# Optimization experiments

Measured on AMD Instinct MI355X. Metric: run time of the kernel, lower is better.

Reference implementation:

```python
import jax, jax.numpy as jnp
import numpy as np

N, E, T, D, A = 50000, 160000, 8192, 32, 6  # nodes, edges, torsions, dim, action_dim


def setup_inputs() -> dict:
    key = jax.random.key(0)
    ks = jax.random.split(key, 16)
    rn = lambda k, s, sc=0.1: jax.random.normal(k, s, jnp.float32) * sc
    return {
        "x": jax.random.normal(ks[0], (N, 3), jnp.float32),
        "edge_index": jax.random.randint(ks[1], (2, E), 0, N),
        "edge_attr": jax.random.uniform(ks[2], (E, 7), dtype=jnp.float32),
        "nonring": jax.random.randint(ks[3], (T, 4), 0, N),
        "lin0_w": rn(ks[4], (3, D)), "lin0_b": jnp.zeros((D,), jnp.float32),
        "nn1_w": rn(ks[5], (7, D)), "nn1_b": jnp.zeros((D,), jnp.float32),
        "nn2_w": rn(ks[6], (D, D * D), 0.02), "nn2_b": jnp.zeros((D * D,), jnp.float32),
        "conv_root": rn(ks[7], (D, D)), "conv_b": jnp.zeros((D,), jnp.float32),
        "gru_w_ih": rn(ks[8], (D, 3 * D)), "gru_w_hh": rn(ks[9], (D, 3 * D)),
        "gru_b_ih": jnp.zeros((3 * D,), jnp.float32), "gru_b_hh": jnp.zeros((3 * D,), jnp.float32),
        "lstm_w_ih": rn(ks[10], (2 * D, 4 * D)), "lstm_w_hh": rn(ks[11], (D, 4 * D)),
        "lstm_b_ih": jnp.zeros((4 * D,), jnp.float32), "lstm_b_hh": jnp.zeros((4 * D,), jnp.float32),
        "lin1_w": rn(ks[12], (6 * D, D)), "lin1_b": jnp.zeros((D,), jnp.float32),
        "lin2_w": rn(ks[13], (D, A)), "lin2_b": jnp.zeros((A,), jnp.float32),
    }


def reference(x, edge_index, edge_attr, nonring,
              lin0_w, lin0_b, nn1_w, nn1_b, nn2_w, nn2_b, conv_root, conv_b,
              gru_w_ih, gru_w_hh, gru_b_ih, gru_b_hh,
              lstm_w_ih, lstm_w_hh, lstm_b_ih, lstm_b_hh,
              lin1_w, lin1_b, lin2_w, lin2_b):
    src, dst = edge_index[0], edge_index[1]
    out = jax.nn.relu(x @ lin0_w + lin0_b)                       # [N, D]
    h = out                                                      # GRU hidden (batch = nodes)
    # Per-edge dim x dim weight matrices (edge_attr is loop-invariant)
    Wedge = (jax.nn.relu(edge_attr @ nn1_w + nn1_b) @ nn2_w + nn2_b).reshape(E, D, D)
    deg = jnp.clip(jax.ops.segment_sum(jnp.ones((E,), jnp.float32), dst, num_segments=N), 1.0)[:, None]
    for _ in range(6):
        # NNConv: gather -> per-edge matvec -> scatter-mean, plus root transform + bias
        msg = jnp.einsum('ei,eio->eo', out[src], Wedge)          # [E, D]
        agg = jax.ops.segment_sum(msg, dst, num_segments=N) / deg
        m = jax.nn.relu(out @ conv_root + agg + conv_b)
        # GRU step (torch gate order r, z, n)
        gx = m @ gru_w_ih + gru_b_ih
        gh = h @ gru_w_hh + gru_b_hh
        r = jax.nn.sigmoid(gx[:, :D] + gh[:, :D])
        z = jax.nn.sigmoid(gx[:, D:2 * D] + gh[:, D:2 * D])
        n = jnp.tanh(gx[:, 2 * D:] + r * gh[:, 2 * D:])
        h = (1.0 - z) * n + z * h
        out = h
    # Set2Set pooling, single graph (B = 1); torch LSTM gate order i, f, g, o
    hl = jnp.zeros((D,), out.dtype)
    cl = jnp.zeros((D,), out.dtype)
    q_star = jnp.zeros((2 * D,), out.dtype)
    for _ in range(6):
        g = q_star @ lstm_w_ih + lstm_b_ih + hl @ lstm_w_hh + lstm_b_hh
        i = jax.nn.sigmoid(g[:D]); f = jax.nn.sigmoid(g[D:2 * D])
        gg = jnp.tanh(g[2 * D:3 * D]); o = jax.nn.sigmoid(g[3 * D:])
        cl = f * cl + i * gg
        hl = o * jnp.tanh(cl)
        q = hl
        a = jax.nn.softmax(out @ q)                              # attention over all nodes
        r_vec = a @ out                                          # [D]
        q_star = jnp.concatenate([q, r_vec])                     # [2D]
    pool = q_star                                                # [2D]
    g4 = out[nonring.reshape(-1)]                                # [4T, D]
    g4 = g4.reshape(4 * D, -1).T                                 # [T, 4D] (faithful view+permute)
    rep = jnp.repeat(pool, g4.shape[0]).reshape(g4.shape[0], -1) # [T, 2D] (repeat_interleave+view)
    cat = jnp.concatenate([g4, rep], axis=1)                     # [T, 6D]
    y = jax.nn.relu(cat @ lin1_w + lin1_b)
    return y @ lin2_w + lin2_b                                   # [T, A]
```

## Files before the change

### kernel.cpp

```cpp
#include <hip/hip_runtime.h>
#include <hip/hip_bf16.h>

#define NN 50000
#define NE 160000
#define NT 8192
#define DD 32
#define AA 6

typedef __attribute__((ext_vector_type(8))) short bf16x8s;
typedef __attribute__((ext_vector_type(4))) float f32x4;

__device__ float g_out[NN * DD];
__device__ float g_msg[NE * DD];
__device__ unsigned int g_h2b[NE * 16];
__device__ int g_src[NE];
__device__ int g_poe[NE];
__device__ unsigned int g_bcnt[NN];
__device__ unsigned int g_row[NN + 1];
__device__ unsigned int g_cur[NN];
__device__ unsigned int g_btot[256], g_boff[256];
__device__ bf16x8s g_w2frag[33 * 2 * 64];
__device__ bf16x8s g_gru_frag[28 * 64];
__device__ float g_hl[DD], g_cl[DD], g_q[DD], g_part[DD + 1];
__device__ unsigned int g_cnt;

__device__ __forceinline__ float sigm(float x) { return 1.0f / (1.0f + __expf(-x)); }
__device__ __forceinline__ float tanhx(float x) { return 1.0f - 2.0f / (__expf(2.0f * x) + 1.0f); }
__device__ __forceinline__ unsigned short f2bf(float f) {
    unsigned int u = __float_as_uint(f);
    u = (u + 0x7fffu + ((u >> 16) & 1u)) >> 16;
    return (unsigned short)u;
}
__device__ __forceinline__ float bflo(unsigned int pk) { return __uint_as_float(pk << 16); }
__device__ __forceinline__ float bfhi(unsigned int pk) { return __uint_as_float(pk & 0xffff0000u); }
__device__ __forceinline__ void fma4(float4& a, float s, const float4 b) {
    a.x = fmaf(s, b.x, a.x); a.y = fmaf(s, b.y, a.y);
    a.z = fmaf(s, b.z, a.z); a.w = fmaf(s, b.w, a.w);
}
#define CVTPK(dst, lo, hi) asm("v_cvt_pk_bf16_f32 %0, %1, %2" : "=v"(dst) : "v"(lo), "v"(hi))

__device__ __forceinline__ void split8(const float* v, bf16x8s& hi, bf16x8s& lo) {
    union U { bf16x8s v; unsigned int u[4]; } H, L;
    CVTPK(H.u[0], v[0], v[1]); CVTPK(H.u[1], v[2], v[3]);
    CVTPK(H.u[2], v[4], v[5]); CVTPK(H.u[3], v[6], v[7]);
    float r[8];
#pragma unroll
    for (int q = 0; q < 4; ++q) {
        r[2 * q]     = v[2 * q]     - bflo(H.u[q]);
        r[2 * q + 1] = v[2 * q + 1] - bfhi(H.u[q]);
    }
    CVTPK(L.u[0], r[0], r[1]); CVTPK(L.u[1], r[2], r[3]);
    CVTPK(L.u[2], r[4], r[5]); CVTPK(L.u[3], r[6], r[7]);
    hi = H.v; lo = L.v;
}

__global__ __launch_bounds__(256) void k_zero() {
    const int n = blockIdx.x * 256 + threadIdx.x;
    if (n < NN) g_bcnt[n] = 0u;
}

__global__ __launch_bounds__(256) void k_hist(const int* __restrict__ ei) {
    const int e = blockIdx.x * 256 + threadIdx.x;
    atomicAdd(&g_bcnt[ei[NE + e]], 1u);
}

__global__ __launch_bounds__(256) void k_scanA() {
    __shared__ unsigned int s[256];
    const int t = threadIdx.x;
    const int idx = blockIdx.x * 256 + t;
    const unsigned int c = (idx < NN) ? g_bcnt[idx] : 0u;
    s[t] = c;
    __syncthreads();
#pragma unroll
    for (int off = 1; off < 256; off <<= 1) {
        const unsigned int o = (t >= off) ? s[t - off] : 0u;
        __syncthreads();
        s[t] += o;
        __syncthreads();
    }
    if (idx < NN) g_row[idx] = s[t] - c;
    if (t == 255) g_btot[blockIdx.x] = s[255];
}

__global__ void k_scanB() {
    __shared__ unsigned int s[256];
    const int t = threadIdx.x;
    const unsigned int c = (t < 196) ? g_btot[t] : 0u;
    s[t] = c;
    __syncthreads();
#pragma unroll
    for (int off = 1; off < 256; off <<= 1) {
        const unsigned int o = (t >= off) ? s[t - off] : 0u;
        __syncthreads();
        s[t] += o;
        __syncthreads();
    }
    if (t < 196) g_boff[t] = s[t] - c;
}

__global__ __launch_bounds__(256) void k_scanC() {
    const int idx = blockIdx.x * 256 + threadIdx.x;
    if (idx < NN) {
        const unsigned int v = g_row[idx] + g_boff[blockIdx.x];
        g_row[idx] = v;
        g_cur[idx] = v;
    }
    if (idx == 0) g_row[NN] = NE;
}

__global__ __launch_bounds__(256) void k_scatter(const int* __restrict__ ei) {
    const int e = blockIdx.x * 256 + threadIdx.x;
    const int d = ei[NE + e];
    const unsigned int pos = atomicAdd(&g_cur[d], 1u);
    g_src[pos] = ei[e];
    g_poe[pos] = e;
}

__global__ __launch_bounds__(256) void k_init(const float* __restrict__ x,
                                              const float* __restrict__ w,
                                              const float* __restrict__ b) {
    const int t = blockIdx.x * 256 + threadIdx.x;
    const int n = t >> 5, d = t & 31;
    float v = b[d];
    v = fmaf(x[n * 3 + 0], w[0 * DD + d], v);
    v = fmaf(x[n * 3 + 1], w[1 * DD + d], v);
    v = fmaf(x[n * 3 + 2], w[2 * DD + d], v);
    g_out[t] = fmaxf(v, 0.f);
}

__global__ __launch_bounds__(256) void k_h2(const float* __restrict__ ea,
                                            const float* __restrict__ w,
                                            const float* __restrict__ b) {
    const int t = blockIdx.x * 256 + threadIdx.x;
    const int p = t >> 4, kp = t & 15;
    const int oe = g_poe[p];
    const int k0 = kp * 2;
    float a0 = b[k0], a1 = b[k0 + 1];
#pragma unroll
    for (int i = 0; i < 7; ++i) {
        const float eav = ea[oe * 7 + i];
        a0 = fmaf(eav, w[i * DD + k0], a0);
        a1 = fmaf(eav, w[i * DD + k0 + 1], a1);
    }
    unsigned int pk;
    CVTPK(pk, fmaxf(a0, 0.f), fmaxf(a1, 0.f));
    g_h2b[t] = pk;
}

__global__ __launch_bounds__(256) void k_w2frag(const float* __restrict__ w2m,
                                                const float* __restrict__ b2m) {
    const int idx = blockIdx.x * 256 + threadIdx.x;
    const int j = idx & 7, l = (idx >> 3) & 63, c = (idx >> 9) & 1, s = idx >> 10;
    const int kk = (l >> 4) * 8 + j;
    const int col = c * 16 + (l & 15);
    const float v = (s == 32) ? b2m[kk * DD + col] : w2m[(32 * s + kk) * DD + col];
    ((unsigned short*)g_w2frag)[idx] = f2bf(v);
}

__global__ __launch_bounds__(256) void k_gfrag(const float* __restrict__ root,
                                               const float* __restrict__ wih,
                                               const float* __restrict__ whh) {
    const int tid = blockIdx.x * 256 + threadIdx.x;
    if (tid >= 28 * 64) return;
    const int lane = tid & 63, f = tid >> 6;
    const float* M; int ncols, c, part;
    if (f < 4)       { M = root; ncols = 32; c = f >> 1;        part = f & 1; }
    else if (f < 16) { M = wih;  ncols = 96; c = (f - 4) >> 1;  part = f & 1; }
    else             { M = whh;  ncols = 96; c = (f - 16) >> 1; part = f & 1; }
    unsigned short out8[8];
#pragma unroll
    for (int j = 0; j < 8; ++j) {
        const int k = (lane >> 4) * 8 + j;
        const float v = M[k * ncols + c * 16 + (lane & 15)];
        const unsigned short hi = f2bf(v);
        out8[j] = (part == 0) ? hi : f2bf(v - __uint_as_float((unsigned int)hi << 16));
    }
    g_gru_frag[f * 64 + lane] = *(bf16x8s*)out8;
}

__global__ __launch_bounds__(256) void k_edge_mfma() {
    const int wid = threadIdx.x >> 6, lane = threadIdx.x & 63;
    const int w = blockIdx.x * 4 + wid;
    const int col = lane & 15, quad = lane >> 4;
    const bf16x8s* __restrict__ B = g_w2frag;

    const bf16x8s bbias0 = B[32 * 128 + lane];
    const bf16x8s bbias1 = B[32 * 128 + 64 + lane];

    float4 u0[2], u1[2];
    unsigned int h2p[2][16];
#pragma unroll
    for (int g = 0; g < 2; ++g) {
        const int e = w * 32 + g * 16 + col;
        const int src = g_src[e];
        u0[g] = *(const float4*)&g_out[src * DD + quad * 8];
        u1[g] = *(const float4*)&g_out[src * DD + quad * 8 + 4];
        *(uint4*)&h2p[g][0]  = *(const uint4*)&g_h2b[e * 16];
        *(uint4*)&h2p[g][4]  = *(const uint4*)&g_h2b[e * 16 + 4];
        *(uint4*)&h2p[g][8]  = *(const uint4*)&g_h2b[e * 16 + 8];
        *(uint4*)&h2p[g][12] = *(const uint4*)&g_h2b[e * 16 + 12];
    }

    union ABu { bf16x8s v; unsigned int u[4]; };
    f32x4 acc[2][2];
#pragma unroll
    for (int g = 0; g < 2; ++g) {
        acc[g][0] = (f32x4){0.f, 0.f, 0.f, 0.f};
        acc[g][1] = (f32x4){0.f, 0.f, 0.f, 0.f};
    }

#define EDGE_STEP(S, B0V, B1V)                                                                   \
    do {                                                                                          \
        _Pragma("unroll")                                                                         \
        for (int g = 0; g < 2; ++g) {                                                             \
            const unsigned int hw = h2p[g][(S) >> 1];                                             \
            const float hs = ((S)&1) ? bfhi(hw) : bflo(hw);                                       \
            ABu A;                                                                                \
            CVTPK(A.u[0], hs * u0[g].x, hs * u0[g].y);                                            \
            CVTPK(A.u[1], hs * u0[g].z, hs * u0[g].w);                                            \
            CVTPK(A.u[2], hs * u1[g].x, hs * u1[g].y);                                            \
            CVTPK(A.u[3], hs * u1[g].z, hs * u1[g].w);                                            \
            acc[g][0] = __builtin_amdgcn_mfma_f32_16x16x32_bf16(A.v, B0V, acc[g][0], 0, 0, 0);    \
            acc[g][1] = __builtin_amdgcn_mfma_f32_16x16x32_bf16(A.v, B1V, acc[g][1], 0, 0, 0);    \
        }                                                                                         \
    } while (0)

    bf16x8s ca0 = B[0 * 128 + lane], cb0 = B[0 * 128 + 64 + lane];
    bf16x8s ca1 = B[1 * 128 + lane], cb1 = B[1 * 128 + 64 + lane];
    bf16x8s ca2 = B[2 * 128 + lane], cb2 = B[2 * 128 + 64 + lane];
    bf16x8s ca3 = B[3 * 128 + lane], cb3 = B[3 * 128 + 64 + lane];
    bf16x8s na0, nb0, na1, nb1, na2, nb2, na3, nb3;

#pragma unroll
    for (int blk = 0; blk < 8; ++blk) {
        if (blk < 7) {
            const int r = blk * 4 + 4;
            na0 = B[(r + 0) * 128 + lane]; nb0 = B[(r + 0) * 128 + 64 + lane];
            na1 = B[(r + 1) * 128 + lane]; nb1 = B[(r + 1) * 128 + 64 + lane];
            na2 = B[(r + 2) * 128 + lane]; nb2 = B[(r + 2) * 128 + 64 + lane];
            na3 = B[(r + 3) * 128 + lane]; nb3 = B[(r + 3) * 128 + 64 + lane];
        }
        EDGE_STEP(blk * 4 + 0, ca0, cb0);
        EDGE_STEP(blk * 4 + 1, ca1, cb1);
        EDGE_STEP(blk * 4 + 2, ca2, cb2);
        EDGE_STEP(blk * 4 + 3, ca3, cb3);
        if (blk < 7) {
            ca0 = na0; cb0 = nb0; ca1 = na1; cb1 = nb1;
            ca2 = na2; cb2 = nb2; ca3 = na3; cb3 = nb3;
        }
    }
#undef EDGE_STEP

    {
#pragma unroll
        for (int g = 0; g < 2; ++g) {
            ABu Au;
            CVTPK(Au.u[0], u0[g].x, u0[g].y); CVTPK(Au.u[1], u0[g].z, u0[g].w);
            CVTPK(Au.u[2], u1[g].x, u1[g].y); CVTPK(Au.u[3], u1[g].z, u1[g].w);
            acc[g][0] = __builtin_amdgcn_mfma_f32_16x16x32_bf16(Au.v, bbias0, acc[g][0], 0, 0, 0);
            acc[g][1] = __builtin_amdgcn_mfma_f32_16x16x32_bf16(Au.v, bbias1, acc[g][1], 0, 0, 0);
        }
    }
#pragma unroll
    for (int g = 0; g < 2; ++g)
#pragma unroll
        for (int r = 0; r < 4; ++r) {
            const int p = w * 32 + g * 16 + quad * 4 + r;
            g_msg[p * DD + col] = acc[g][0][r];
            g_msg[p * DD + 16 + col] = acc[g][1][r];
        }
}

__global__ __launch_bounds__(256) void k_node_mfma(const float* __restrict__ cb,
                                                   const float* __restrict__ bih,
                                                   const float* __restrict__ bhh) {
    __shared__ float sm[4][16 * 36];
    const int wid = threadIdx.x >> 6, lane = threadIdx.x & 63;
    const int nt = blockIdx.x * 4 + wid;
    if (nt >= NN / 16) return;
    const int nb = nt * 16;
    const int col = lane & 15, quad = lane >> 4;
    const bf16x8s* FB = g_gru_frag;

    float hv8[8];
    *(float4*)&hv8[0] = *(const float4*)&g_out[(nb + col) * DD + quad * 8];
    *(float4*)&hv8[4] = *(const float4*)&g_out[(nb + col) * DD + quad * 8 + 4];
    bf16x8s hAh, hAl; split8(hv8, hAh, hAl);

    float aggv0[4], aggv1[4], invr[4];
#pragma unroll
    for (int r = 0; r < 4; ++r) {
        const int node = nb + quad * 4 + r;
        const unsigned int e0 = g_row[node], e1 = g_row[node + 1];
        float a0 = 0.f, a1 = 0.f;
        for (unsigned int e = e0; e < e1; ++e) {
            a0 += g_msg[e * DD + col];
            a1 += g_msg[e * DD + 16 + col];
        }
        aggv0[r] = a0; aggv1[r] = a1;
        invr[r] = 1.0f / fmaxf((float)(e1 - e0), 1.0f);
    }

#pragma unroll
    for (int c = 0; c < 2; ++c) {
        const float cbv = cb[c * 16 + col];
        f32x4 aM;
#pragma unroll
        for (int r = 0; r < 4; ++r)
            aM[r] = fmaf((c == 0) ? aggv0[r] : aggv1[r], invr[r], cbv);
        const bf16x8s Bh = FB[(c * 2 + 0) * 64 + lane];
        const bf16x8s Bl = FB[(c * 2 + 1) * 64 + lane];
        aM = __builtin_amdgcn_mfma_f32_16x16x32_bf16(hAh, Bh, aM, 0, 0, 0);
        aM = __builtin_amdgcn_mfma_f32_16x16x32_bf16(hAl, Bh, aM, 0, 0, 0);
        aM = __builtin_amdgcn_mfma_f32_16x16x32_bf16(hAh, Bl, aM, 0, 0, 0);
#pragma unroll
        for (int r = 0; r < 4; ++r)
            sm[wid][(quad * 4 + r) * 36 + c * 16 + col] = fmaxf(aM[r], 0.f);
    }

    float mv8[8];
    *(float4*)&mv8[0] = *(const float4*)&sm[wid][col * 36 + quad * 8];
    *(float4*)&mv8[4] = *(const float4*)&sm[wid][col * 36 + quad * 8 + 4];
    bf16x8s mAh, mAl; split8(mv8, mAh, mAl);

    f32x4 R[2], Z[2], XN[2], HN[2];
#pragma unroll
    for (int c = 0; c < 6; ++c) {
        const float bx = bih[c * 16 + col], bh = bhh[c * 16 + col];
        f32x4 aX = {bx, bx, bx, bx}, aH = {bh, bh, bh, bh};
        const bf16x8s WIhf = FB[(4 + c * 2) * 64 + lane];
        const bf16x8s WIlf = FB[(5 + c * 2) * 64 + lane];
        const bf16x8s WHhf = FB[(16 + c * 2) * 64 + lane];
        const bf16x8s WHlf = FB[(17 + c * 2) * 64 + lane];
        aX = __builtin_amdgcn_mfma_f32_16x16x32_bf16(mAh, WIhf, aX, 0, 0, 0);
        aX = __builtin_amdgcn_mfma_f32_16x16x32_bf16(mAl, WIhf, aX, 0, 0, 0);
        aX = __builtin_amdgcn_mfma_f32_16x16x32_bf16(mAh, WIlf, aX, 0, 0, 0);
        aH = __builtin_amdgcn_mfma_f32_16x16x32_bf16(hAh, WHhf, aH, 0, 0, 0);
        aH = __builtin_amdgcn_mfma_f32_16x16x32_bf16(hAl, WHhf, aH, 0, 0, 0);
        aH = __builtin_amdgcn_mfma_f32_16x16x32_bf16(hAh, WHlf, aH, 0, 0, 0);
        if (c < 2) {
#pragma unroll
            for (int r = 0; r < 4; ++r) R[c][r] = sigm(aX[r] + aH[r]);
        } else if (c < 4) {
#pragma unroll
            for (int r = 0; r < 4; ++r) Z[c - 2][r] = sigm(aX[r] + aH[r]);
        } else {
            XN[c - 4] = aX; HN[c - 4] = aH;
        }
    }
#pragma unroll
    for (int c = 0; c < 2; ++c)
#pragma unroll
        for (int r = 0; r < 4; ++r) {
            const int addr = (nb + quad * 4 + r) * DD + c * 16 + col;
            const float nv = tanhx(XN[c][r] + R[c][r] * HN[c][r]);
            const float hv = g_out[addr];
            g_out[addr] = (1.f - Z[c][r]) * nv + Z[c][r] * hv;
        }
}

__global__ void k_lstm0(const float* __restrict__ bih, const float* __restrict__ bhh) {
    __shared__ float gg[128];
    const int t = threadIdx.x;
    gg[t] = bih[t] + bhh[t];
    __syncthreads();
    if (t < DD) {
        const float ig = sigm(gg[t]), fg = sigm(gg[DD + t]);
        const float g2 = tanhx(gg[2 * DD + t]), og = sigm(gg[3 * DD + t]);
        const float cc = ig * g2;
        g_cl[t] = cc; const float hn = og * tanhx(cc); g_hl[t] = hn; g_q[t] = hn;
        (void)fg;
    }
    if (t >= DD && t < 2 * DD + 1) g_part[t - DD] = 0.f;
    if (t == 0) g_cnt = 0u;
}

__global__ __launch_bounds__(256) void k_att_f(const float* __restrict__ wih,
                                               const float* __restrict__ whh,
                                               const float* __restrict__ bih,
                                               const float* __restrict__ bhh,
                                               const int dolstm) {
    __shared__ float sq[DD];
    __shared__ float red[4][DD + 1];
    __shared__ int slast;
    __shared__ float qs[64], shl[DD], gg[128];
    if (threadIdx.x < DD) sq[threadIdx.x] = g_q[threadIdx.x];
    __syncthreads();
    float pe = 0.f;
    float pv[DD];
#pragma unroll
    for (int i = 0; i < DD; ++i) pv[i] = 0.f;
    for (int n = blockIdx.x * blockDim.x + threadIdx.x; n < NN; n += gridDim.x * blockDim.x) {
        float row[DD];
#pragma unroll
        for (int q = 0; q < 8; ++q) *(float4*)&row[4 * q] = *(const float4*)&g_out[n * DD + 4 * q];
        float dot = 0.f;
#pragma unroll
        for (int i = 0; i < DD; ++i) dot = fmaf(row[i], sq[i], dot);
        const float e = __expf(dot);
        pe += e;
#pragma unroll
        for (int i = 0; i < DD; ++i) pv[i] = fmaf(e, row[i], pv[i]);
    }
#pragma unroll
    for (int off = 32; off > 0; off >>= 1) {
        pe += __shfl_down(pe, off, 64);
#pragma unroll
        for (int i = 0; i < DD; ++i) pv[i] += __shfl_down(pv[i], off, 64);
    }
    const int wid = threadIdx.x >> 6, lane = threadIdx.x & 63;
    if (lane == 0) {
        red[wid][0] = pe;
#pragma unroll
        for (int i = 0; i < DD; ++i) red[wid][1 + i] = pv[i];
    }
    __syncthreads();
    if (threadIdx.x < DD + 1) {
        const float s = red[0][threadIdx.x] + red[1][threadIdx.x] + red[2][threadIdx.x] + red[3][threadIdx.x];
        atomicAdd(&g_part[threadIdx.x], s);
    }
    __threadfence();
    __syncthreads();
    if (threadIdx.x == 0) {
        const unsigned int o = atomicAdd(&g_cnt, 1u);
        slast = (o == (unsigned int)(gridDim.x - 1)) ? 1 : 0;
    }
    __syncthreads();
    if (!slast) return;
    __threadfence();
    const int t = threadIdx.x;
    if (dolstm) {
        if (t < DD) { qs[t] = g_q[t]; shl[t] = g_hl[t]; }
        else if (t < 64) qs[t] = g_part[1 + t - DD] / g_part[0];
        __syncthreads();
        if (t < 128) {
            float acc = bih[t] + bhh[t];
            for (int i = 0; i < 64; ++i) acc = fmaf(qs[i], wih[i * 128 + t], acc);
            for (int i = 0; i < DD; ++i) acc = fmaf(shl[i], whh[i * 128 + t], acc);
            gg[t] = acc;
        }
        __syncthreads();
        if (t < DD) {
            const float ig = sigm(gg[t]), fg = sigm(gg[DD + t]);
            const float g2 = tanhx(gg[2 * DD + t]), og = sigm(gg[3 * DD + t]);
            const float cc = fmaf(fg, g_cl[t], ig * g2);
            g_cl[t] = cc; const float hn = og * tanhx(cc); g_hl[t] = hn; g_q[t] = hn;
        }
        if (t >= DD && t < 2 * DD + 1) g_part[t - DD] = 0.f;
    }
    if (t == 0) g_cnt = 0u;
}

__global__ __launch_bounds__(128) void k_readout(const int* __restrict__ nr,
                                                 const float* __restrict__ w1,
                                                 const float* __restrict__ b1,
                                                 const float* __restrict__ w2,
                                                 const float* __restrict__ b2,
                                                 float* __restrict__ yout) {
    __shared__ float sw1[192 * DD];
    __shared__ float sS1[DD];
    __shared__ float sw2[DD * AA];
    __shared__ float sb1[DD];
    __shared__ float sb2[AA];
    __shared__ float sred[32 * DD];
    for (int i = threadIdx.x; i < 192 * DD; i += 128) sw1[i] = w1[i];
    for (int i = threadIdx.x; i < DD * AA; i += 128) sw2[i] = w2[i];
    if (threadIdx.x < DD) sb1[threadIdx.x] = b1[threadIdx.x];
    if (threadIdx.x >= DD && threadIdx.x < DD + AA) sb2[threadIdx.x - DD] = b2[threadIdx.x - DD];
    __syncthreads();
    if (threadIdx.x < DD) {
        float s = 0.f;
        for (int c = 0; c < 64; ++c) s += sw1[(128 + c) * DD + threadIdx.x];
        sS1[threadIdx.x] = s;
    }
    __syncthreads();
    const int g = blockIdx.x;
    const int t0 = g * 32;
    const int f = threadIdx.x & 31;
    const int slice = threadIdx.x >> 5;
    const int rowbase = g >> 2, col = g & 3;
    float4 acc[8];
#pragma unroll
    for (int q = 0; q < 8; ++q) acc[q] = make_float4(0.f, 0.f, 0.f, 0.f);
    for (int pp = 0; pp < 32; ++pp) {
        const int p = slice * 32 + pp;
        const int node = nr[(p * 64 + rowbase) * 4 + col];
        const float v = g_out[node * DD + f];
#pragma unroll
        for (int q = 0; q < 8; ++q) fma4(acc[q], v, *(const float4*)&sw1[p * DD + 4 * q]);
    }
#pragma unroll
    for (int q = 0; q < 8; ++q) {
        acc[q].x += __shfl_xor(acc[q].x, 32, 64);
        acc[q].y += __shfl_xor(acc[q].y, 32, 64);
        acc[q].z += __shfl_xor(acc[q].z, 32, 64);
        acc[q].w += __shfl_xor(acc[q].w, 32, 64);
    }
    if (threadIdx.x >= 64 && threadIdx.x < 96) {
#pragma unroll
        for (int q = 0; q < 8; ++q) *(float4*)&sred[f * DD + 4 * q] = acc[q];
    }
    __syncthreads();
    if (threadIdx.x < 32) {
        const int pidx = g >> 2;
        const float poolv = (pidx < DD) ? g_q[pidx] : (g_part[1 + (pidx - DD)] / g_part[0]);
        float y[AA];
#pragma unroll
        for (int a = 0; a < AA; ++a) y[a] = sb2[a];
#pragma unroll
        for (int q = 0; q < 8; ++q) {
            const float4 o = *(const float4*)&sred[f * DD + 4 * q];
            const float vals[4] = {acc[q].x + o.x, acc[q].y + o.y, acc[q].z + o.z, acc[q].w + o.w};
#pragma unroll
            for (int cc = 0; cc < 4; ++cc) {
                const int d = 4 * q + cc;
                const float ad = fmaxf(fmaf(poolv, sS1[d], sb1[d]) + vals[cc], 0.f);
#pragma unroll
                for (int a = 0; a < AA; ++a) y[a] = fmaf(ad, sw2[d * AA + a], y[a]);
            }
        }
#pragma unroll
        for (int a = 0; a < AA; ++a) yout[(t0 + f) * AA + a] = y[a];
    }
}

extern "C" void kernel_launch(void* const* d_in, const int* in_sizes, int n_in,
                              void* d_out, int out_size, void* d_ws, size_t ws_size,
                              hipStream_t stream) {
    (void)in_sizes; (void)n_in; (void)out_size; (void)d_ws; (void)ws_size;
    const float* x        = (const float*)d_in[0];
    const int*   ei       = (const int*)d_in[1];
    const float* ea       = (const float*)d_in[2];
    const int*   nonring  = (const int*)d_in[3];
    const float* lin0_w   = (const float*)d_in[4];
    const float* lin0_b   = (const float*)d_in[5];
    const float* nn1_w    = (const float*)d_in[6];
    const float* nn1_b    = (const float*)d_in[7];
    const float* nn2_w    = (const float*)d_in[8];
    const float* nn2_b    = (const float*)d_in[9];
    const float* conv_root= (const float*)d_in[10];
    const float* conv_b   = (const float*)d_in[11];
    const float* gru_w_ih = (const float*)d_in[12];
    const float* gru_w_hh = (const float*)d_in[13];
    const float* gru_b_ih = (const float*)d_in[14];
    const float* gru_b_hh = (const float*)d_in[15];
    const float* lstm_w_ih= (const float*)d_in[16];
    const float* lstm_w_hh= (const float*)d_in[17];
    const float* lstm_b_ih= (const float*)d_in[18];
    const float* lstm_b_hh= (const float*)d_in[19];
    const float* lin1_w   = (const float*)d_in[20];
    const float* lin1_b   = (const float*)d_in[21];
    const float* lin2_w   = (const float*)d_in[22];
    const float* lin2_b   = (const float*)d_in[23];
    float* out = (float*)d_out;

    k_zero<<<196, 256, 0, stream>>>();
    k_hist<<<NE / 256, 256, 0, stream>>>(ei);
    k_scanA<<<196, 256, 0, stream>>>();
    k_scanB<<<1, 256, 0, stream>>>();
    k_scanC<<<196, 256, 0, stream>>>();
    k_scatter<<<NE / 256, 256, 0, stream>>>(ei);

    k_init<<<(NN * DD) / 256, 256, 0, stream>>>(x, lin0_w, lin0_b);
    k_h2<<<(NE * 16) / 256, 256, 0, stream>>>(ea, nn1_w, nn1_b);
    k_w2frag<<<132, 256, 0, stream>>>(nn2_w, nn2_b);
    k_gfrag<<<7, 256, 0, stream>>>(conv_root, gru_w_ih, gru_w_hh);
    for (int it = 0; it < 6; ++it) {
        k_edge_mfma<<<1250, 256, 0, stream>>>();
        k_node_mfma<<<(NN / 16 + 3) / 4, 256, 0, stream>>>(conv_b, gru_b_ih, gru_b_hh);
    }
    k_lstm0<<<1, 128, 0, stream>>>(lstm_b_ih, lstm_b_hh);
    for (int s = 0; s < 6; ++s) {
        k_att_f<<<196, 256, 0, stream>>>(lstm_w_ih, lstm_w_hh, lstm_b_ih, lstm_b_hh, (s < 5) ? 1 : 0);
    }
    k_readout<<<256, 128, 0, stream>>>(nonring, lin1_w, lin1_b, lin2_w, lin2_b, out);
}
```

Before: 440.6 us.

## Fuse edge message computation into node GRU kernel with ping-pong node buffers

Merges the per-edge NNConv message MFMA kernel into the per-node aggregation/GRU kernel. Each wave now walks the CSR edge range of its 16-node tile in chunks of 16 edges, computes messages into LDS and accumulates them directly, which removes the global g_msg write and read each iteration. Because messages now read node state while other blocks update it, the node state is double-buffered (g_out/g_out2) with the iteration parity picking the buffers. The trade-off is fewer waves and less independent work per wave, one edge group instead of two, and idle lanes in partial chunks.

Measured after the change: 649.7 us. +47.5%, slower.

```diff
diff --git a/kernel.cpp b/kernel.cpp
--- a/kernel.cpp
+++ b/kernel.cpp
@@ -11,7 +11,7 @@
 typedef __attribute__((ext_vector_type(4))) float f32x4;
 
 __device__ float g_out[NN * DD];
-__device__ float g_msg[NE * DD];
+__device__ float g_out2[NN * DD];
 __device__ unsigned int g_h2b[NE * 16];
 __device__ int g_src[NE];
 __device__ int g_poe[NE];
@@ -178,128 +178,123 @@
     g_gru_frag[f * 64 + lane] = *(bf16x8s*)out8;
 }
 
-__global__ __launch_bounds__(256) void k_edge_mfma() {
-    const int wid = threadIdx.x >> 6, lane = threadIdx.x & 63;
-    const int w = blockIdx.x * 4 + wid;
-    const int col = lane & 15, quad = lane >> 4;
-    const bf16x8s* __restrict__ B = g_w2frag;
-
-    const bf16x8s bbias0 = B[32 * 128 + lane];
-    const bf16x8s bbias1 = B[32 * 128 + 64 + lane];
-
-    float4 u0[2], u1[2];
-    unsigned int h2p[2][16];
-#pragma unroll
-    for (int g = 0; g < 2; ++g) {
-        const int e = w * 32 + g * 16 + col;
-        const int src = g_src[e];
-        u0[g] = *(const float4*)&g_out[src * DD + quad * 8];
-        u1[g] = *(const float4*)&g_out[src * DD + quad * 8 + 4];
-        *(uint4*)&h2p[g][0]  = *(const uint4*)&g_h2b[e * 16];
-        *(uint4*)&h2p[g][4]  = *(const uint4*)&g_h2b[e * 16 + 4];
-        *(uint4*)&h2p[g][8]  = *(const uint4*)&g_h2b[e * 16 + 8];
-        *(uint4*)&h2p[g][12] = *(const uint4*)&g_h2b[e * 16 + 12];
-    }
-
-    union ABu { bf16x8s v; unsigned int u[4]; };
-    f32x4 acc[2][2];
-#pragma unroll
-    for (int g = 0; g < 2; ++g) {
-        acc[g][0] = (f32x4){0.f, 0.f, 0.f, 0.f};
-        acc[g][1] = (f32x4){0.f, 0.f, 0.f, 0.f};
-    }
-
-#define EDGE_STEP(S, B0V, B1V)                                                                   \
-    do {                                                                                          \
-        _Pragma("unroll")                                                                         \
-        for (int g = 0; g < 2; ++g) {                                                             \
-            const unsigned int hw = h2p[g][(S) >> 1];                                             \
-            const float hs = ((S)&1) ? bfhi(hw) : bflo(hw);                                       \
-            ABu A;                                                                                \
-            CVTPK(A.u[0], hs * u0[g].x, hs * u0[g].y);                                            \
-            CVTPK(A.u[1], hs * u0[g].z, hs * u0[g].w);                                            \
-            CVTPK(A.u[2], hs * u1[g].x, hs * u1[g].y);                                            \
-            CVTPK(A.u[3], hs * u1[g].z, hs * u1[g].w);                                            \
-            acc[g][0] = __builtin_amdgcn_mfma_f32_16x16x32_bf16(A.v, B0V, acc[g][0], 0, 0, 0);    \
-            acc[g][1] = __builtin_amdgcn_mfma_f32_16x16x32_bf16(A.v, B1V, acc[g][1], 0, 0, 0);    \
-        }                                                                                         \
-    } while (0)
-
-    bf16x8s ca0 = B[0 * 128 + lane], cb0 = B[0 * 128 + 64 + lane];
-    bf16x8s ca1 = B[1 * 128 + lane], cb1 = B[1 * 128 + 64 + lane];
-    bf16x8s ca2 = B[2 * 128 + lane], cb2 = B[2 * 128 + 64 + lane];
-    bf16x8s ca3 = B[3 * 128 + lane], cb3 = B[3 * 128 + 64 + lane];
-    bf16x8s na0, nb0, na1, nb1, na2, nb2, na3, nb3;
-
-#pragma unroll
-    for (int blk = 0; blk < 8; ++blk) {
-        if (blk < 7) {
-            const int r = blk * 4 + 4;
-            na0 = B[(r + 0) * 128 + lane]; nb0 = B[(r + 0) * 128 + 64 + lane];
-            na1 = B[(r + 1) * 128 + lane]; nb1 = B[(r + 1) * 128 + 64 + lane];
-            na2 = B[(r + 2) * 128 + lane]; nb2 = B[(r + 2) * 128 + 64 + lane];
-            na3 = B[(r + 3) * 128 + lane]; nb3 = B[(r + 3) * 128 + 64 + lane];
-        }
-        EDGE_STEP(blk * 4 + 0, ca0, cb0);
-        EDGE_STEP(blk * 4 + 1, ca1, cb1);
-        EDGE_STEP(blk * 4 + 2, ca2, cb2);
-        EDGE_STEP(blk * 4 + 3, ca3, cb3);
-        if (blk < 7) {
-            ca0 = na0; cb0 = nb0; ca1 = na1; cb1 = nb1;
-            ca2 = na2; cb2 = nb2; ca3 = na3; cb3 = nb3;
-        }
-    }
-#undef EDGE_STEP
-
-    {
-#pragma unroll
-        for (int g = 0; g < 2; ++g) {
-            ABu Au;
-            CVTPK(Au.u[0], u0[g].x, u0[g].y); CVTPK(Au.u[1], u0[g].z, u0[g].w);
-            CVTPK(Au.u[2], u1[g].x, u1[g].y); CVTPK(Au.u[3], u1[g].z, u1[g].w);
-            acc[g][0] = __builtin_amdgcn_mfma_f32_16x16x32_bf16(Au.v, bbias0, acc[g][0], 0, 0, 0);
-            acc[g][1] = __builtin_amdgcn_mfma_f32_16x16x32_bf16(Au.v, bbias1, acc[g][1], 0, 0, 0);
-        }
-    }
-#pragma unroll
-    for (int g = 0; g < 2; ++g)
-#pragma unroll
-        for (int r = 0; r < 4; ++r) {
-            const int p = w * 32 + g * 16 + quad * 4 + r;
-            g_msg[p * DD + col] = acc[g][0][r];
-            g_msg[p * DD + 16 + col] = acc[g][1][r];
-        }
-}
-
-__global__ __launch_bounds__(256) void k_node_mfma(const float* __restrict__ cb,
-                                                   const float* __restrict__ bih,
-                                                   const float* __restrict__ bhh) {
+__global__ __launch_bounds__(256) void k_fused(const int it,
+                                               const float* __restrict__ cb,
+                                               const float* __restrict__ bih,
+                                               const float* __restrict__ bhh) {
     __shared__ float sm[4][16 * 36];
+    __shared__ float smsg[4][16 * 32];
     const int wid = threadIdx.x >> 6, lane = threadIdx.x & 63;
     const int nt = blockIdx.x * 4 + wid;
     if (nt >= NN / 16) return;
+    const float* __restrict__ cur = (it & 1) ? g_out2 : g_out;
+    float* __restrict__ nxt = (it & 1) ? g_out : g_out2;
     const int nb = nt * 16;
     const int col = lane & 15, quad = lane >> 4;
+    const bf16x8s* __restrict__ B = g_w2frag;
     const bf16x8s* FB = g_gru_frag;
+    float* smt = sm[wid];
+    float* smm = smsg[wid];
 
     float hv8[8];
-    *(float4*)&hv8[0] = *(const float4*)&g_out[(nb + col) * DD + quad * 8];
-    *(float4*)&hv8[4] = *(const float4*)&g_out[(nb + col) * DD + quad * 8 + 4];
+    *(float4*)&hv8[0] = *(const float4*)&cur[(nb + col) * DD + quad * 8];
+    *(float4*)&hv8[4] = *(const float4*)&cur[(nb + col) * DD + quad * 8 + 4];
     bf16x8s hAh, hAl; split8(hv8, hAh, hAl);
 
-    float aggv0[4], aggv1[4], invr[4];
+    unsigned int nr0[4], nr1[4];
 #pragma unroll
     for (int r = 0; r < 4; ++r) {
         const int node = nb + quad * 4 + r;
-        const unsigned int e0 = g_row[node], e1 = g_row[node + 1];
-        float a0 = 0.f, a1 = 0.f;
-        for (unsigned int e = e0; e < e1; ++e) {
-            a0 += g_msg[e * DD + col];
-            a1 += g_msg[e * DD + 16 + col];
-        }
-        aggv0[r] = a0; aggv1[r] = a1;
-        invr[r] = 1.0f / fmaxf((float)(e1 - e0), 1.0f);
-    }
+        nr0[r] = g_row[node];
+        nr1[r] = g_row[node + 1];
+    }
+    const unsigned int e0 = g_row[nb], e1 = g_row[nb + 16];
+
+    const bf16x8s bbias0 = B[32 * 128 + lane];
+    const bf16x8s bbias1 = B[32 * 128 + 64 + lane];
+
+    union ABu { bf16x8s v; unsigned int u[4]; };
+    float agg0[4] = {0.f, 0.f, 0.f, 0.f};
+    float agg1[4] = {0.f, 0.f, 0.f, 0.f};
+
+    for (unsigned int ec = e0; ec < e1; ec += 16) {
+        const int e = min((int)(ec + col), NE - 1);
+        const int src = g_src[e];
+        const float4 u0 = *(const float4*)&cur[src * DD + quad * 8];
+        const float4 u1 = *(const float4*)&cur[src * DD + quad * 8 + 4];
+        unsigned int h2p[16];
+        *(uint4*)&h2p[0]  = *(const uint4*)&g_h2b[(size_t)e * 16];
+        *(uint4*)&h2p[4]  = *(const uint4*)&g_h2b[(size_t)e * 16 + 4];
+        *(uint4*)&h2p[8]  = *(const uint4*)&g_h2b[(size_t)e * 16 + 8];
+        *(uint4*)&h2p[12] = *(const uint4*)&g_h2b[(size_t)e * 16 + 12];
+
+        f32x4 acc0 = {0.f, 0.f, 0.f, 0.f};
+        f32x4 acc1 = {0.f, 0.f, 0.f, 0.f};
+
+#define EDGE_STEP(S, B0V, B1V)                                                                 \
+    do {                                                                                        \
+        const unsigned int hw = h2p[(S) >> 1];                                                  \
+        const float hs = ((S)&1) ? bfhi(hw) : bflo(hw);                                         \
+        ABu A;                                                                                  \
+        CVTPK(A.u[0], hs * u0.x, hs * u0.y);                                                    \
+        CVTPK(A.u[1], hs * u0.z, hs * u0.w);                                                    \
+        CVTPK(A.u[2], hs * u1.x, hs * u1.y);                                                    \
+        CVTPK(A.u[3], hs * u1.z, hs * u1.w);                                                    \
+        acc0 = __builtin_amdgcn_mfma_f32_16x16x32_bf16(A.v, B0V, acc0, 0, 0, 0);                \
+        acc1 = __builtin_amdgcn_mfma_f32_16x16x32_bf16(A.v, B1V, acc1, 0, 0, 0);                \
+    } while (0)
+
+        bf16x8s ca0 = B[0 * 128 + lane], cb0 = B[0 * 128 + 64 + lane];
+        bf16x8s ca1 = B[1 * 128 + lane], cb1 = B[1 * 128 + 64 + lane];
+        bf16x8s ca2 = B[2 * 128 + lane], cb2 = B[2 * 128 + 64 + lane];
+        bf16x8s ca3 = B[3 * 128 + lane], cb3 = B[3 * 128 + 64 + lane];
+        bf16x8s na0, nb0, na1, nb1, na2, nb2, na3, nb3;
+#pragma unroll
+        for (int blk = 0; blk < 8; ++blk) {
+            if (blk < 7) {
+                const int r = blk * 4 + 4;
+                na0 = B[(r + 0) * 128 + lane]; nb0 = B[(r + 0) * 128 + 64 + lane];
+                na1 = B[(r + 1) * 128 + lane]; nb1 = B[(r + 1) * 128 + 64 + lane];
+                na2 = B[(r + 2) * 128 + lane]; nb2 = B[(r + 2) * 128 + 64 + lane];
+                na3 = B[(r + 3) * 128 + lane]; nb3 = B[(r + 3) * 128 + 64 + lane];
+            }
+            EDGE_STEP(blk * 4 + 0, ca0, cb0);
+            EDGE_STEP(blk * 4 + 1, ca1, cb1);
+            EDGE_STEP(blk * 4 + 2, ca2, cb2);
+            EDGE_STEP(blk * 4 + 3, ca3, cb3);
+            if (blk < 7) {
+                ca0 = na0; cb0 = nb0; ca1 = na1; cb1 = nb1;
+                ca2 = na2; cb2 = nb2; ca3 = na3; cb3 = nb3;
+            }
+        }
+#undef EDGE_STEP
+        {
+            ABu Au;
+            CVTPK(Au.u[0], u0.x, u0.y); CVTPK(Au.u[1], u0.z, u0.w);
+            CVTPK(Au.u[2], u1.x, u1.y); CVTPK(Au.u[3], u1.z, u1.w);
+            acc0 = __builtin_amdgcn_mfma_f32_16x16x32_bf16(Au.v, bbias0, acc0, 0, 0, 0);
+            acc1 = __builtin_amdgcn_mfma_f32_16x16x32_bf16(Au.v, bbias1, acc1, 0, 0, 0);
+        }
+#pragma unroll
+        for (int r = 0; r < 4; ++r) {
+            smm[(quad * 4 + r) * 32 + col] = acc0[r];
+            smm[(quad * 4 + r) * 32 + 16 + col] = acc1[r];
+        }
+#pragma unroll
+        for (int r = 0; r < 4; ++r) {
+            const int lo = (int)max(nr0[r], ec) - (int)ec;
+            const int hi = (int)min(nr1[r], ec + 16u) - (int)ec;
+            for (int s = lo; s < hi; ++s) {
+                agg0[r] += smm[s * 32 + col];
+                agg1[r] += smm[s * 32 + 16 + col];
+            }
+        }
+    }
+
+    float invr[4];
+#pragma unroll
+    for (int r = 0; r < 4; ++r)
+        invr[r] = 1.0f / fmaxf((float)(nr1[r] - nr0[r]), 1.0f);
 
 #pragma unroll
     for (int c = 0; c < 2; ++c) {
@@ -307,7 +302,7 @@
         f32x4 aM;
 #pragma unroll
         for (int r = 0; r < 4; ++r)
-            aM[r] = fmaf((c == 0) ? aggv0[r] : aggv1[r], invr[r], cbv);
+            aM[r] = fmaf((c == 0) ? agg0[r] : agg1[r], invr[r], cbv);
         const bf16x8s Bh = FB[(c * 2 + 0) * 64 + lane];
         const bf16x8s Bl = FB[(c * 2 + 1) * 64 + lane];
         aM = __builtin_amdgcn_mfma_f32_16x16x32_bf16(hAh, Bh, aM, 0, 0, 0);
@@ -315,12 +310,12 @@
         aM = __builtin_amdgcn_mfma_f32_16x16x32_bf16(hAh, Bl, aM, 0, 0, 0);
 #pragma unroll
         for (int r = 0; r < 4; ++r)
-            sm[wid][(quad * 4 + r) * 36 + c * 16 + col] = fmaxf(aM[r], 0.f);
+            smt[(quad * 4 + r) * 36 + c * 16 + col] = fmaxf(aM[r], 0.f);
     }
 
     float mv8[8];
-    *(float4*)&mv8[0] = *(const float4*)&sm[wid][col * 36 + quad * 8];
-    *(float4*)&mv8[4] = *(const float4*)&sm[wid][col * 36 + quad * 8 + 4];
+    *(float4*)&mv8[0] = *(const float4*)&smt[col * 36 + quad * 8];
+    *(float4*)&mv8[4] = *(const float4*)&smt[col * 36 + quad * 8 + 4];
     bf16x8s mAh, mAl; split8(mv8, mAh, mAl);
 
     f32x4 R[2], Z[2], XN[2], HN[2];
@@ -354,8 +349,8 @@
         for (int r = 0; r < 4; ++r) {
             const int addr = (nb + quad * 4 + r) * DD + c * 16 + col;
             const float nv = tanhx(XN[c][r] + R[c][r] * HN[c][r]);
-            const float hv = g_out[addr];
-            g_out[addr] = (1.f - Z[c][r]) * nv + Z[c][r] * hv;
+            const float hv = cur[addr];
+            nxt[addr] = (1.f - Z[c][r]) * nv + Z[c][r] * hv;
         }
 }
 
@@ -365,11 +360,10 @@
     gg[t] = bih[t] + bhh[t];
     __syncthreads();
     if (t < DD) {
-        const float ig = sigm(gg[t]), fg = sigm(gg[DD + t]);
+        const float ig = sigm(gg[t]);
         const float g2 = tanhx(gg[2 * DD + t]), og = sigm(gg[3 * DD + t]);
         const float cc = ig * g2;
         g_cl[t] = cc; const float hn = og * tanhx(cc); g_hl[t] = hn; g_q[t] = hn;
-        (void)fg;
     }
     if (t >= DD && t < 2 * DD + 1) g_part[t - DD] = 0.f;
     if (t == 0) g_cnt = 0u;
@@ -565,9 +559,9 @@
     k_h2<<<(NE * 16) / 256, 256, 0, stream>>>(ea, nn1_w, nn1_b);
     k_w2frag<<<132, 256, 0, stream>>>(nn2_w, nn2_b);
     k_gfrag<<<7, 256, 0, stream>>>(conv_root, gru_w_ih, gru_w_hh);
+
     for (int it = 0; it < 6; ++it) {
-        k_edge_mfma<<<1250, 256, 0, stream>>>();
-        k_node_mfma<<<(NN / 16 + 3) / 4, 256, 0, stream>>>(conv_b, gru_b_ih, gru_b_hh);
+        k_fused<<<(NN / 16 + 3) / 4, 256, 0, stream>>>(it, conv_b, gru_b_ih, gru_b_hh);
     }
     k_lstm0<<<1, 128, 0, stream>>>(lstm_b_ih, lstm_b_hh);
     for (int s = 0; s < 6; ++s) {
```

## Fuse setup kernels into one prep kernel and stage edge messages through LDS

Applied to the files above, without the earlier changes.

Four small setup kernels (zeroing, node init, weight fragment packing, LSTM init) are merged into a single launch to cut launch overhead. The node kernel's per-node scalar CSR aggregation loop is replaced by cooperative, coalesced float4 loads of each 16-edge chunk of the tile's contiguous edge range into per-wave shared memory, followed by per-node summation from LDS. This targets poorly coalesced, serial global reads in the scatter-mean, at the cost of an extra LDS buffer and a chunk loop over the whole tile range. There is no explicit wave-level barrier between the LDS writes and reads, which relies on lockstep wave execution.

After: 406.5 us. 1.08x faster.

```diff
diff --git a/kernel.cpp b/kernel.cpp
--- a/kernel.cpp
+++ b/kernel.cpp
@@ -54,9 +54,58 @@
     hi = H.v; lo = L.v;
 }
 
-__global__ __launch_bounds__(256) void k_zero() {
-    const int n = blockIdx.x * 256 + threadIdx.x;
-    if (n < NN) g_bcnt[n] = 0u;
+__global__ __launch_bounds__(256) void k_prep0(const float* __restrict__ x,
+                                               const float* __restrict__ l0w,
+                                               const float* __restrict__ l0b,
+                                               const float* __restrict__ w2m,
+                                               const float* __restrict__ b2m,
+                                               const float* __restrict__ root,
+                                               const float* __restrict__ wih,
+                                               const float* __restrict__ whh,
+                                               const float* __restrict__ lbih,
+                                               const float* __restrict__ lbhh) {
+    const int t = blockIdx.x * 256 + threadIdx.x;
+    {
+        const int n = t >> 5, d = t & 31;
+        float v = l0b[d];
+        v = fmaf(x[n * 3 + 0], l0w[0 * DD + d], v);
+        v = fmaf(x[n * 3 + 1], l0w[1 * DD + d], v);
+        v = fmaf(x[n * 3 + 2], l0w[2 * DD + d], v);
+        g_out[t] = fmaxf(v, 0.f);
+    }
+    if (t < NN) g_bcnt[t] = 0u;
+    if (t < 33 * 2 * 64 * 8) {
+        const int j = t & 7, l = (t >> 3) & 63, c = (t >> 9) & 1, s = t >> 10;
+        const int kk = (l >> 4) * 8 + j;
+        const int col = c * 16 + (l & 15);
+        const float v = (s == 32) ? b2m[kk * DD + col] : w2m[(32 * s + kk) * DD + col];
+        ((unsigned short*)g_w2frag)[t] = f2bf(v);
+    }
+    if (t < 28 * 64) {
+        const int lane = t & 63, f = t >> 6;
+        const float* M; int ncols, c, part;
+        if (f < 4)       { M = root; ncols = 32; c = f >> 1;        part = f & 1; }
+        else if (f < 16) { M = wih;  ncols = 96; c = (f - 4) >> 1;  part = f & 1; }
+        else             { M = whh;  ncols = 96; c = (f - 16) >> 1; part = f & 1; }
+        unsigned short out8[8];
+#pragma unroll
+        for (int j = 0; j < 8; ++j) {
+            const int k = (lane >> 4) * 8 + j;
+            const float v = M[k * ncols + c * 16 + (lane & 15)];
+            const unsigned short hi = f2bf(v);
+            out8[j] = (part == 0) ? hi : f2bf(v - __uint_as_float((unsigned int)hi << 16));
+        }
+        g_gru_frag[f * 64 + lane] = *(bf16x8s*)out8;
+    }
+    if (t < DD) {
+        const float ig = sigm(lbih[t] + lbhh[t]);
+        const float g2 = tanhx(lbih[2 * DD + t] + lbhh[2 * DD + t]);
+        const float og = sigm(lbih[3 * DD + t] + lbhh[3 * DD + t]);
+        const float cc = ig * g2;
+        g_cl[t] = cc; const float hn = og * tanhx(cc); g_hl[t] = hn; g_q[t] = hn;
+    }
+    if (t >= DD && t < 2 * DD + 1 + DD) { if (t - DD <= 2 * DD) g_part[t - DD] = 0.f; }
+    if (t == 1793) g_cnt = 0u;
 }
 
 __global__ __launch_bounds__(256) void k_hist(const int* __restrict__ ei) {
@@ -114,18 +163,6 @@
     const unsigned int pos = atomicAdd(&g_cur[d], 1u);
     g_src[pos] = ei[e];
     g_poe[pos] = e;
-}
-
-__global__ __launch_bounds__(256) void k_init(const float* __restrict__ x,
-                                              const float* __restrict__ w,
-                                              const float* __restrict__ b) {
-    const int t = blockIdx.x * 256 + threadIdx.x;
-    const int n = t >> 5, d = t & 31;
-    float v = b[d];
-    v = fmaf(x[n * 3 + 0], w[0 * DD + d], v);
-    v = fmaf(x[n * 3 + 1], w[1 * DD + d], v);
-    v = fmaf(x[n * 3 + 2], w[2 * DD + d], v);
-    g_out[t] = fmaxf(v, 0.f);
 }
 
 __global__ __launch_bounds__(256) void k_h2(const float* __restrict__ ea,
@@ -145,37 +182,6 @@
     unsigned int pk;
     CVTPK(pk, fmaxf(a0, 0.f), fmaxf(a1, 0.f));
     g_h2b[t] = pk;
-}
-
-__global__ __launch_bounds__(256) void k_w2frag(const float* __restrict__ w2m,
-                                                const float* __restrict__ b2m) {
-    const int idx = blockIdx.x * 256 + threadIdx.x;
-    const int j = idx & 7, l = (idx >> 3) & 63, c = (idx >> 9) & 1, s = idx >> 10;
-    const int kk = (l >> 4) * 8 + j;
-    const int col = c * 16 + (l & 15);
-    const float v = (s == 32) ? b2m[kk * DD + col] : w2m[(32 * s + kk) * DD + col];
-    ((unsigned short*)g_w2frag)[idx] = f2bf(v);
-}
-
-__global__ __launch_bounds__(256) void k_gfrag(const float* __restrict__ root,
-                                               const float* __restrict__ wih,
-                                               const float* __restrict__ whh) {
-    const int tid = blockIdx.x * 256 + threadIdx.x;
-    if (tid >= 28 * 64) return;
-    const int lane = tid & 63, f = tid >> 6;
-    const float* M; int ncols, c, part;
-    if (f < 4)       { M = root; ncols = 32; c = f >> 1;        part = f & 1; }
-    else if (f < 16) { M = wih;  ncols = 96; c = (f - 4) >> 1;  part = f & 1; }
-    else             { M = whh;  ncols = 96; c = (f - 16) >> 1; part = f & 1; }
-    unsigned short out8[8];
-#pragma unroll
-    for (int j = 0; j < 8; ++j) {
-        const int k = (lane >> 4) * 8 + j;
-        const float v = M[k * ncols + c * 16 + (lane & 15)];
-        const unsigned short hi = f2bf(v);
-        out8[j] = (part == 0) ? hi : f2bf(v - __uint_as_float((unsigned int)hi << 16));
-    }
-    g_gru_frag[f * 64 + lane] = *(bf16x8s*)out8;
 }
 
 __global__ __launch_bounds__(256) void k_edge_mfma() {
@@ -275,31 +281,53 @@
                                                    const float* __restrict__ bih,
                                                    const float* __restrict__ bhh) {
     __shared__ float sm[4][16 * 36];
+    __shared__ float smsg[4][16 * 32];
     const int wid = threadIdx.x >> 6, lane = threadIdx.x & 63;
     const int nt = blockIdx.x * 4 + wid;
     if (nt >= NN / 16) return;
     const int nb = nt * 16;
     const int col = lane & 15, quad = lane >> 4;
     const bf16x8s* FB = g_gru_frag;
+    float* smt = sm[wid];
+    float* smm = smsg[wid];
 
     float hv8[8];
     *(float4*)&hv8[0] = *(const float4*)&g_out[(nb + col) * DD + quad * 8];
     *(float4*)&hv8[4] = *(const float4*)&g_out[(nb + col) * DD + quad * 8 + 4];
     bf16x8s hAh, hAl; split8(hv8, hAh, hAl);
 
-    float aggv0[4], aggv1[4], invr[4];
+    unsigned int nr0[4], nr1[4];
 #pragma unroll
     for (int r = 0; r < 4; ++r) {
         const int node = nb + quad * 4 + r;
-        const unsigned int e0 = g_row[node], e1 = g_row[node + 1];
-        float a0 = 0.f, a1 = 0.f;
-        for (unsigned int e = e0; e < e1; ++e) {
-            a0 += g_msg[e * DD + col];
-            a1 += g_msg[e * DD + 16 + col];
-        }
-        aggv0[r] = a0; aggv1[r] = a1;
-        invr[r] = 1.0f / fmaxf((float)(e1 - e0), 1.0f);
-    }
+        nr0[r] = g_row[node];
+        nr1[r] = g_row[node + 1];
+    }
+    const unsigned int e0t = g_row[nb], e1t = g_row[nb + 16];
+
+    float agg0[4] = {0.f, 0.f, 0.f, 0.f};
+    float agg1[4] = {0.f, 0.f, 0.f, 0.f};
+    for (unsigned int ec = e0t; ec < e1t; ec += 16) {
+        const int idx = min((int)ec * 32 + lane * 8, NE * 32 - 8);
+        const float4 v0 = *(const float4*)&g_msg[idx];
+        const float4 v1 = *(const float4*)&g_msg[idx + 4];
+        *(float4*)&smm[lane * 8] = v0;
+        *(float4*)&smm[lane * 8 + 4] = v1;
+#pragma unroll
+        for (int r = 0; r < 4; ++r) {
+            const int lo = (int)max(nr0[r], ec) - (int)ec;
+            const int hi = (int)min(nr1[r], ec + 16u) - (int)ec;
+            for (int s = lo; s < hi; ++s) {
+                agg0[r] += smm[s * 32 + col];
+                agg1[r] += smm[s * 32 + 16 + col];
+            }
+        }
+    }
+
+    float invr[4];
+#pragma unroll
+    for (int r = 0; r < 4; ++r)
+        invr[r] = 1.0f / fmaxf((float)(nr1[r] - nr0[r]), 1.0f);
 
 #pragma unroll
     for (int c = 0; c < 2; ++c) {
@@ -307,7 +335,7 @@
         f32x4 aM;
 #pragma unroll
         for (int r = 0; r < 4; ++r)
-            aM[r] = fmaf((c == 0) ? aggv0[r] : aggv1[r], invr[r], cbv);
+            aM[r] = fmaf((c == 0) ? agg0[r] : agg1[r], invr[r], cbv);
         const bf16x8s Bh = FB[(c * 2 + 0) * 64 + lane];
         const bf16x8s Bl = FB[(c * 2 + 1) * 64 + lane];
         aM = __builtin_amdgcn_mfma_f32_16x16x32_bf16(hAh, Bh, aM, 0, 0, 0);
@@ -315,12 +343,12 @@
         aM = __builtin_amdgcn_mfma_f32_16x16x32_bf16(hAh, Bl, aM, 0, 0, 0);
 #pragma unroll
         for (int r = 0; r < 4; ++r)
-            sm[wid][(quad * 4 + r) * 36 + c * 16 + col] = fmaxf(aM[r], 0.f);
+            smt[(quad * 4 + r) * 36 + c * 16 + col] = fmaxf(aM[r], 0.f);
     }
 
     float mv8[8];
-    *(float4*)&mv8[0] = *(const float4*)&sm[wid][col * 36 + quad * 8];
-    *(float4*)&mv8[4] = *(const float4*)&sm[wid][col * 36 + quad * 8 + 4];
+    *(float4*)&mv8[0] = *(const float4*)&smt[col * 36 + quad * 8];
+    *(float4*)&mv8[4] = *(const float4*)&smt[col * 36 + quad * 8 + 4];
     bf16x8s mAh, mAl; split8(mv8, mAh, mAl);
 
     f32x4 R[2], Z[2], XN[2], HN[2];
@@ -357,22 +385,6 @@
             const float hv = g_out[addr];
             g_out[addr] = (1.f - Z[c][r]) * nv + Z[c][r] * hv;
         }
-}
-
-__global__ void k_lstm0(const float* __restrict__ bih, const float* __restrict__ bhh) {
-    __shared__ float gg[128];
-    const int t = threadIdx.x;
-    gg[t] = bih[t] + bhh[t];
-    __syncthreads();
-    if (t < DD) {
-        const float ig = sigm(gg[t]), fg = sigm(gg[DD + t]);
-        const float g2 = tanhx(gg[2 * DD + t]), og = sigm(gg[3 * DD + t]);
-        const float cc = ig * g2;
-        g_cl[t] = cc; const float hn = og * tanhx(cc); g_hl[t] = hn; g_q[t] = hn;
-        (void)fg;
-    }
-    if (t >= DD && t < 2 * DD + 1) g_part[t - DD] = 0.f;
-    if (t == 0) g_cnt = 0u;
 }
 
 __global__ __launch_bounds__(256) void k_att_f(const float* __restrict__ wih,
@@ -554,22 +566,20 @@
     const float* lin2_b   = (const float*)d_in[23];
     float* out = (float*)d_out;
 
-    k_zero<<<196, 256, 0, stream>>>();
+    k_prep0<<<(NN * DD) / 256, 256, 0, stream>>>(x, lin0_w, lin0_b, nn2_w, nn2_b,
+                                                 conv_root, gru_w_ih, gru_w_hh,
+                                                 lstm_b_ih, lstm_b_hh);
     k_hist<<<NE / 256, 256, 0, stream>>>(ei);
     k_scanA<<<196, 256, 0, stream>>>();
     k_scanB<<<1, 256, 0, stream>>>();
     k_scanC<<<196, 256, 0, stream>>>();
     k_scatter<<<NE / 256, 256, 0, stream>>>(ei);
-
-    k_init<<<(NN * DD) / 256, 256, 0, stream>>>(x, lin0_w, lin0_b);
     k_h2<<<(NE * 16) / 256, 256, 0, stream>>>(ea, nn1_w, nn1_b);
-    k_w2frag<<<132, 256, 0, stream>>>(nn2_w, nn2_b);
-    k_gfrag<<<7, 256, 0, stream>>>(conv_root, gru_w_ih, gru_w_hh);
+
     for (int it = 0; it < 6; ++it) {
         k_edge_mfma<<<1250, 256, 0, stream>>>();
         k_node_mfma<<<(NN / 16 + 3) / 4, 256, 0, stream>>>(conv_b, gru_b_ih, gru_b_hh);
     }
-    k_lstm0<<<1, 128, 0, stream>>>(lstm_b_ih, lstm_b_hh);
     for (int s = 0; s < 6; ++s) {
         k_att_f<<<196, 256, 0, stream>>>(lstm_w_ih, lstm_w_hh, lstm_b_ih, lstm_b_hh, (s < 5) ? 1 : 0);
     }
```
